# Kernel tuning notes

Hardware: AMD Instinct MI355X
Metric: run time of the kernel (lower is better)

The kernel has to match this reference:

```python
import jax, jax.numpy as jnp
import numpy as np

NCLASSES = 4
FG_THRESH = 0.5
MEANS = jnp.array([0.0, 0.0, 0.0, 0.0], dtype=jnp.float32)
STDS = jnp.array([0.1, 0.1, 0.2, 0.2], dtype=jnp.float32)
BBOX_INSIDE_W = jnp.array([1.0, 1.0, 1.0, 1.0], dtype=jnp.float32)


def _bbox_overlaps(boxes, gt):
    # boxes: (B,M,4), gt: (B,K,4) -> IoU (B,M,K), faithful to bbox_overlaps_batch
    aw = boxes[..., 2] - boxes[..., 0] + 1.0
    ah = boxes[..., 3] - boxes[..., 1] + 1.0
    gw = gt[..., 2] - gt[..., 0] + 1.0
    gh = gt[..., 3] - gt[..., 1] + 1.0
    area_a = aw * ah                      # (B,M)
    area_g = gw * gh                      # (B,K)
    ix1 = jnp.maximum(boxes[:, :, None, 0], gt[:, None, :, 0])
    iy1 = jnp.maximum(boxes[:, :, None, 1], gt[:, None, :, 1])
    ix2 = jnp.minimum(boxes[:, :, None, 2], gt[:, None, :, 2])
    iy2 = jnp.minimum(boxes[:, :, None, 3], gt[:, None, :, 3])
    iw = jnp.clip(ix2 - ix1 + 1.0, 0.0)
    ih = jnp.clip(iy2 - iy1 + 1.0, 0.0)
    inter = iw * ih                       # (B,M,K)
    ov = inter / (area_a[:, :, None] + area_g[:, None, :] - inter)
    gt_zero = (gw == 1.0) & (gh == 1.0)   # zero-area (padding) gt boxes
    an_zero = (aw == 1.0) & (ah == 1.0)
    ov = jnp.where(gt_zero[:, None, :], 0.0, ov)
    ov = jnp.where(an_zero[:, :, None], -1.0, ov)
    return ov


def _bbox_transform(ex, gt):
    ew = ex[..., 2] - ex[..., 0] + 1.0
    eh = ex[..., 3] - ex[..., 1] + 1.0
    ecx = ex[..., 0] + 0.5 * ew
    ecy = ex[..., 1] + 0.5 * eh
    gw = gt[..., 2] - gt[..., 0] + 1.0
    gh = gt[..., 3] - gt[..., 1] + 1.0
    gcx = gt[..., 0] + 0.5 * gw
    gcy = gt[..., 1] + 0.5 * gh
    dx = (gcx - ecx) / ew
    dy = (gcy - ecy) / eh
    dw = jnp.log(gw / ew)
    dh = jnp.log(gh / eh)
    return jnp.stack([dx, dy, dw, dh], axis=-1)


def setup_inputs() -> dict:
    key = jax.random.key(0)
    B, N, K = 16, 8192, 128
    ks = jax.random.split(key, 9)
    # valid proposal boxes inside an ~1242x375 (KITTI-like) image
    x1 = jax.random.uniform(ks[0], (B, N)) * 1000.0
    y1 = jax.random.uniform(ks[1], (B, N)) * 300.0
    bw = jax.random.uniform(ks[2], (B, N)) * 200.0 + 4.0
    bh = jax.random.uniform(ks[3], (B, N)) * 150.0 + 4.0
    all_rois = jnp.concatenate(
        [jnp.zeros((B, N, 1), jnp.float32),
         jnp.stack([x1, y1, x1 + bw, y1 + bh], axis=-1)], axis=-1)
    gx1 = jax.random.uniform(ks[4], (B, K)) * 1000.0
    gy1 = jax.random.uniform(ks[5], (B, K)) * 300.0
    gw = jax.random.uniform(ks[6], (B, K)) * 200.0 + 8.0
    gh = jax.random.uniform(ks[7], (B, K)) * 150.0 + 8.0
    cls = jax.random.randint(ks[8], (B, K), 1, NCLASSES).astype(jnp.float32)
    gt_boxes = jnp.stack([gx1, gy1, gx1 + gw, gy1 + gh, cls], axis=-1)
    return {"all_rois": all_rois, "gt_boxes": gt_boxes}


def reference(all_rois, gt_boxes):
    B = all_rois.shape[0]
    dt = all_rois.dtype
    # append gt boxes as extra rois: (0, x1, y1, x2, y2)
    gt_append = jnp.concatenate(
        [jnp.zeros_like(gt_boxes[..., :1]), gt_boxes[..., :4]], axis=-1)
    rois = jnp.concatenate([all_rois, gt_append], axis=1)   # (B,M,5)
    M = rois.shape[1]

    ov = _bbox_overlaps(rois[..., 1:5], gt_boxes[..., :4])  # (B,M,K)
    max_ov = ov.max(axis=2)                                 # (B,M)
    gt_assign = jnp.argmax(ov, axis=2)                      # (B,M)
    labels_all = jnp.take_along_axis(gt_boxes[..., 4], gt_assign, axis=1)

    # focal-loss path: fg = ov >= thresh, keep order = [fg asc, bg asc]
    fg = max_ov >= FG_THRESH
    order = jnp.argsort(jnp.where(fg, 0, 1).astype(jnp.int32), axis=1, stable=True)
    fg_count = fg.sum(axis=1)                               # (B,)
    pos = jnp.arange(M)[None, :]

    labels_perm = jnp.take_along_axis(labels_all, order, axis=1)
    labels_batch = jnp.where(pos < fg_count[:, None], labels_perm, 0.0)

    rois_perm = jnp.take_along_axis(rois, order[..., None], axis=1)
    rois_batch = rois_perm.at[..., 0].set(
        jnp.broadcast_to(jnp.arange(B, dtype=dt)[:, None], (B, M)))

    ga_perm = jnp.take_along_axis(gt_assign, order, axis=1)
    gt_rois = jnp.take_along_axis(gt_boxes, ga_perm[..., None], axis=1)  # (B,M,5)

    targets = _bbox_transform(rois_batch[..., 1:5], gt_rois[..., :4])
    targets = (targets - MEANS) / STDS
    bbox_targets = jnp.where((labels_batch > 0)[..., None], targets, 0.0)

    # focal inside weights in ORIGINAL roi order (as in the source), bg zeroed
    focal_w = jnp.where(fg, (1.0 - max_ov) ** 2, 0.0)       # (B,M)
    bbox_inside_weights = jnp.broadcast_to(focal_w[..., None], (B, M, 4))
    bbox_outside_weights = (bbox_inside_weights > 0).astype(dt)

    return (rois_batch, labels_batch, bbox_targets,
            bbox_inside_weights, bbox_outside_weights)
```

## Files before the change

### kernel.cpp

```cpp
#include <hip/hip_runtime.h>
#include <math.h>

#define BB 16
#define NN 8192
#define KK 128
#define MM (NN + KK)
#define NCHUNK ((MM + 255) / 256)

__global__ __launch_bounds__(256) void ptl_phase1(
    const float* __restrict__ all_rois,
    const float* __restrict__ gt_boxes,
    int* __restrict__ fg_flags,
    int* __restrict__ gt_assign,
    int* __restrict__ chunk_counts,
    float* __restrict__ out_inside,
    float* __restrict__ out_outside)
{
    __shared__ float4 s_box[KK];
    __shared__ int    s_wcnt[4];

    const int b   = blockIdx.y;
    const int tid = threadIdx.x;

    if (tid < KK) {
        const float* g = gt_boxes + ((size_t)b * KK + tid) * 5;
        float gx1 = g[0], gy1 = g[1], gx2 = g[2], gy2 = g[3];
        float gw = gx2 - gx1 + 1.0f, gh = gy2 - gy1 + 1.0f;
        bool z = (gw == 1.0f) && (gh == 1.0f);
        s_box[tid] = z ? make_float4(1e30f, 1e30f, -1e30f, -1e30f)
                       : make_float4(gx1, gy1, gx2 + 1.0f, gy2 + 1.0f);
    }
    __syncthreads();

    const int i = blockIdx.x * 256 + tid;
    const bool valid = (i < MM);

    float x1 = 0.f, y1 = 0.f, x2 = 0.f, y2 = 0.f;
    if (valid) {
        if (i < NN) {
            const float* p = all_rois + ((size_t)b * NN + i) * 5;
            x1 = p[1]; y1 = p[2]; x2 = p[3]; y2 = p[4];
        } else {
            const float* p = gt_boxes + ((size_t)b * KK + (i - NN)) * 5;
            x1 = p[0]; y1 = p[1]; x2 = p[2]; y2 = p[3];
        }
    }
    const float X2p = x2 + 1.0f, Y2p = y2 + 1.0f;
    const float aw = X2p - x1, ah = Y2p - y1;
    const float area_a = aw * ah;

    float best = -1e30f;
    int besti = 0;
    #pragma unroll 4
    for (int k = 0; k < KK; ++k) {
        float4 g = s_box[k];
        float iw = fmaxf(fminf(X2p, g.z) - fmaxf(x1, g.x), 0.0f);
        float ih = fmaxf(fminf(Y2p, g.w) - fmaxf(y1, g.y), 0.0f);
        float inter = iw * ih;
        float area_g = (g.z - g.x) * (g.w - g.y);
        float ov = inter / (area_a + area_g - inter);
        if (ov > best) { best = ov; besti = k; }
    }
    if (aw == 1.0f && ah == 1.0f) { best = -1.0f; besti = 0; }

    const bool fg = valid && (best >= 0.5f);

    unsigned long long m = __ballot(fg ? 1 : 0);
    if ((tid & 63) == 0) s_wcnt[tid >> 6] = __popcll(m);
    __syncthreads();
    if (tid == 0)
        chunk_counts[b * NCHUNK + blockIdx.x] =
            s_wcnt[0] + s_wcnt[1] + s_wcnt[2] + s_wcnt[3];

    if (!valid) return;
    const size_t idx = (size_t)b * MM + i;
    fg_flags[idx]  = fg ? 1 : 0;
    gt_assign[idx] = besti;

    const float om = 1.0f - best;
    const float w  = fg ? om * om : 0.0f;
    const float ow = (w > 0.0f) ? 1.0f : 0.0f;
    ((float4*)out_inside)[idx]  = make_float4(w, w, w, w);
    ((float4*)out_outside)[idx] = make_float4(ow, ow, ow, ow);
}

__global__ __launch_bounds__(256) void ptl_phase2(
    const float* __restrict__ all_rois,
    const float* __restrict__ gt_boxes,
    const int* __restrict__ fg_flags,
    const int* __restrict__ gt_assign,
    const int* __restrict__ chunk_counts,
    float* __restrict__ out_rois,
    float* __restrict__ out_labels,
    float* __restrict__ out_targets)
{
    __shared__ float s_gt[KK * 5];
    __shared__ int   s_cnt[NCHUNK];
    __shared__ int   s_w[4];

    const int b   = blockIdx.y;
    const int cx  = blockIdx.x;
    const int tid = threadIdx.x;

    for (int t = tid; t < KK * 5; t += 256)
        s_gt[t] = gt_boxes[(size_t)b * KK * 5 + t];
    if (tid < NCHUNK)
        s_cnt[tid] = chunk_counts[b * NCHUNK + tid];
    __syncthreads();

    int base = 0, total = 0;
    for (int c = 0; c < NCHUNK; ++c) {
        int v = s_cnt[c];
        total += v;
        if (c < cx) base += v;
    }

    const int i = cx * 256 + tid;
    const bool valid = (i < MM);
    int f = 0, a = 0;
    if (valid) {
        const size_t idx = (size_t)b * MM + i;
        f = fg_flags[idx];
        a = gt_assign[idx];
    }

    const int lane = tid & 63, wv = tid >> 6;
    unsigned long long m = __ballot(f);
    const int lp = __popcll(m & ((1ull << lane) - 1ull));
    if (lane == 0) s_w[wv] = __popcll(m);
    __syncthreads();
    int we = 0;
    for (int w2 = 0; w2 < wv; ++w2) we += s_w[w2];
    const int fgBefore = base + we + lp;

    if (!valid) return;
    const int p = f ? fgBefore : (total + i - fgBefore);

    float x1, y1, x2, y2;
    if (i < NN) {
        const float* q = all_rois + ((size_t)b * NN + i) * 5;
        x1 = q[1]; y1 = q[2]; x2 = q[3]; y2 = q[4];
    } else {
        const float* q = gt_boxes + ((size_t)b * KK + (i - NN)) * 5;
        x1 = q[0]; y1 = q[1]; x2 = q[2]; y2 = q[3];
    }

    float* rp = out_rois + ((size_t)b * MM + p) * 5;
    rp[0] = (float)b;
    rp[1] = x1; rp[2] = y1; rp[3] = x2; rp[4] = y2;

    float lbl = 0.f, t0 = 0.f, t1 = 0.f, t2 = 0.f, t3 = 0.f;
    if (f) {
        lbl = s_gt[a * 5 + 4];
        if (lbl > 0.0f) {
            const float gx1 = s_gt[a * 5 + 0], gy1 = s_gt[a * 5 + 1];
            const float gx2 = s_gt[a * 5 + 2], gy2 = s_gt[a * 5 + 3];
            const float ew = x2 - x1 + 1.0f, eh = y2 - y1 + 1.0f;
            const float ecx = x1 + 0.5f * ew, ecy = y1 + 0.5f * eh;
            const float gw = gx2 - gx1 + 1.0f, gh = gy2 - gy1 + 1.0f;
            const float gcx = gx1 + 0.5f * gw, gcy = gy1 + 0.5f * gh;
            t0 = ((gcx - ecx) / ew) / 0.1f;
            t1 = ((gcy - ecy) / eh) / 0.1f;
            t2 = logf(gw / ew) / 0.2f;
            t3 = logf(gh / eh) / 0.2f;
        }
    }
    out_labels[(size_t)b * MM + p] = lbl;
    float* tp = out_targets + ((size_t)b * MM + p) * 4;
    tp[0] = t0; tp[1] = t1; tp[2] = t2; tp[3] = t3;
}

extern "C" void kernel_launch(void* const* d_in, const int* in_sizes, int n_in,
                              void* d_out, int out_size, void* d_ws, size_t ws_size,
                              hipStream_t stream) {
    const float* all_rois = (const float*)d_in[0];
    const float* gt_boxes = (const float*)d_in[1];

    float* out = (float*)d_out;
    float* out_rois    = out;
    float* out_labels  = out_rois    + (size_t)BB * MM * 5;
    float* out_targets = out_labels  + (size_t)BB * MM;
    float* out_inside  = out_targets + (size_t)BB * MM * 4;
    float* out_outside = out_inside  + (size_t)BB * MM * 4;

    int* fg_flags     = (int*)d_ws;
    int* gt_assign    = fg_flags  + (size_t)BB * MM;
    int* chunk_counts = gt_assign + (size_t)BB * MM;

    dim3 grid(NCHUNK, BB);
    ptl_phase1<<<grid, 256, 0, stream>>>(all_rois, gt_boxes, fg_flags, gt_assign,
                                         chunk_counts, out_inside, out_outside);
    ptl_phase2<<<grid, 256, 0, stream>>>(all_rois, gt_boxes, fg_flags, gt_assign,
                                         chunk_counts, out_rois, out_labels,
                                         out_targets);
}
```

Measured before the change: 83.30 us.

## Fuse IoU/assignment and compaction phases into one cooperative kernel with grid sync

Merges the two kernels into a single cooperative launch that uses a grid-wide barrier between computing per-chunk foreground counts and doing the compacted scatter. Each thread keeps its box coordinates, best IoU and assigned gt index in registers across the barrier. This removes the fg_flags and gt_assign workspace round trip, the second read of the ROIs and gt boxes, and one kernel launch. In exchange it pays for a grid sync and depends on all 528 blocks being co-resident, which cooperative launch enforces.

```diff
diff --git a/kernel.cpp b/kernel.cpp
--- a/kernel.cpp
+++ b/kernel.cpp
@@ -1,4 +1,5 @@
 #include <hip/hip_runtime.h>
+#include <hip/hip_cooperative_groups.h>
 #include <math.h>
 
 #define BB 16
@@ -7,19 +8,25 @@
 #define MM (NN + KK)
 #define NCHUNK ((MM + 255) / 256)
 
-__global__ __launch_bounds__(256) void ptl_phase1(
+namespace cg = cooperative_groups;
+
+__global__ __launch_bounds__(256) void ptl_fused(
     const float* __restrict__ all_rois,
     const float* __restrict__ gt_boxes,
-    int* __restrict__ fg_flags,
-    int* __restrict__ gt_assign,
     int* __restrict__ chunk_counts,
+    float* __restrict__ out_rois,
+    float* __restrict__ out_labels,
+    float* __restrict__ out_targets,
     float* __restrict__ out_inside,
     float* __restrict__ out_outside)
 {
     __shared__ float4 s_box[KK];
-    __shared__ int    s_wcnt[4];
+    __shared__ float  s_lbl[KK];
+    __shared__ int    s_w[4];
+    __shared__ int    s_cnt[NCHUNK];
 
     const int b   = blockIdx.y;
+    const int cx  = blockIdx.x;
     const int tid = threadIdx.x;
 
     if (tid < KK) {
@@ -29,10 +36,11 @@
         bool z = (gw == 1.0f) && (gh == 1.0f);
         s_box[tid] = z ? make_float4(1e30f, 1e30f, -1e30f, -1e30f)
                        : make_float4(gx1, gy1, gx2 + 1.0f, gy2 + 1.0f);
+        s_lbl[tid] = g[4];
     }
     __syncthreads();
 
-    const int i = blockIdx.x * 256 + tid;
+    const int i = cx * 256 + tid;
     const bool valid = (i < MM);
 
     float x1 = 0.f, y1 = 0.f, x2 = 0.f, y2 = 0.f;
@@ -65,49 +73,36 @@
 
     const bool fg = valid && (best >= 0.5f);
 
+    const int lane = tid & 63, wv = tid >> 6;
     unsigned long long m = __ballot(fg ? 1 : 0);
-    if ((tid & 63) == 0) s_wcnt[tid >> 6] = __popcll(m);
+    const int lp = __popcll(m & ((1ull << lane) - 1ull));
+    if (lane == 0) s_w[wv] = __popcll(m);
     __syncthreads();
-    if (tid == 0)
-        chunk_counts[b * NCHUNK + blockIdx.x] =
-            s_wcnt[0] + s_wcnt[1] + s_wcnt[2] + s_wcnt[3];
+    if (tid == 0) {
+        int s = s_w[0] + s_w[1] + s_w[2] + s_w[3];
+        __hip_atomic_store(&chunk_counts[b * NCHUNK + cx], s,
+                           __ATOMIC_RELAXED, __HIP_MEMORY_SCOPE_AGENT);
+    }
+    int we = 0;
+    for (int w2 = 0; w2 < wv; ++w2) we += s_w[w2];
+    const int inChunkExcl = we + lp;
 
-    if (!valid) return;
-    const size_t idx = (size_t)b * MM + i;
-    fg_flags[idx]  = fg ? 1 : 0;
-    gt_assign[idx] = besti;
+    if (valid) {
+        const size_t idx = (size_t)b * MM + i;
+        const float om = 1.0f - best;
+        const float w  = fg ? om * om : 0.0f;
+        const float ow = (w > 0.0f) ? 1.0f : 0.0f;
+        ((float4*)out_inside)[idx]  = make_float4(w, w, w, w);
+        ((float4*)out_outside)[idx] = make_float4(ow, ow, ow, ow);
+    }
 
-    const float om = 1.0f - best;
-    const float w  = fg ? om * om : 0.0f;
-    const float ow = (w > 0.0f) ? 1.0f : 0.0f;
-    ((float4*)out_inside)[idx]  = make_float4(w, w, w, w);
-    ((float4*)out_outside)[idx] = make_float4(ow, ow, ow, ow);
-}
+    __threadfence();
+    cg::this_grid().sync();
 
-__global__ __launch_bounds__(256) void ptl_phase2(
-    const float* __restrict__ all_rois,
-    const float* __restrict__ gt_boxes,
-    const int* __restrict__ fg_flags,
-    const int* __restrict__ gt_assign,
-    const int* __restrict__ chunk_counts,
-    float* __restrict__ out_rois,
-    float* __restrict__ out_labels,
-    float* __restrict__ out_targets)
-{
-    __shared__ float s_gt[KK * 5];
-    __shared__ int   s_cnt[NCHUNK];
-    __shared__ int   s_w[4];
-
-    const int b   = blockIdx.y;
-    const int cx  = blockIdx.x;
-    const int tid = threadIdx.x;
-
-    for (int t = tid; t < KK * 5; t += 256)
-        s_gt[t] = gt_boxes[(size_t)b * KK * 5 + t];
     if (tid < NCHUNK)
-        s_cnt[tid] = chunk_counts[b * NCHUNK + tid];
+        s_cnt[tid] = __hip_atomic_load(&chunk_counts[b * NCHUNK + tid],
+                                       __ATOMIC_RELAXED, __HIP_MEMORY_SCOPE_AGENT);
     __syncthreads();
-
     int base = 0, total = 0;
     for (int c = 0; c < NCHUNK; ++c) {
         int v = s_cnt[c];
@@ -115,50 +110,23 @@
         if (c < cx) base += v;
     }
 
-    const int i = cx * 256 + tid;
-    const bool valid = (i < MM);
-    int f = 0, a = 0;
-    if (valid) {
-        const size_t idx = (size_t)b * MM + i;
-        f = fg_flags[idx];
-        a = gt_assign[idx];
-    }
-
-    const int lane = tid & 63, wv = tid >> 6;
-    unsigned long long m = __ballot(f);
-    const int lp = __popcll(m & ((1ull << lane) - 1ull));
-    if (lane == 0) s_w[wv] = __popcll(m);
-    __syncthreads();
-    int we = 0;
-    for (int w2 = 0; w2 < wv; ++w2) we += s_w[w2];
-    const int fgBefore = base + we + lp;
-
     if (!valid) return;
-    const int p = f ? fgBefore : (total + i - fgBefore);
-
-    float x1, y1, x2, y2;
-    if (i < NN) {
-        const float* q = all_rois + ((size_t)b * NN + i) * 5;
-        x1 = q[1]; y1 = q[2]; x2 = q[3]; y2 = q[4];
-    } else {
-        const float* q = gt_boxes + ((size_t)b * KK + (i - NN)) * 5;
-        x1 = q[0]; y1 = q[1]; x2 = q[2]; y2 = q[3];
-    }
+    const int fgBefore = base + inChunkExcl;
+    const int p = fg ? fgBefore : (total + i - fgBefore);
 
     float* rp = out_rois + ((size_t)b * MM + p) * 5;
     rp[0] = (float)b;
     rp[1] = x1; rp[2] = y1; rp[3] = x2; rp[4] = y2;
 
     float lbl = 0.f, t0 = 0.f, t1 = 0.f, t2 = 0.f, t3 = 0.f;
-    if (f) {
-        lbl = s_gt[a * 5 + 4];
+    if (fg) {
+        lbl = s_lbl[besti];
         if (lbl > 0.0f) {
-            const float gx1 = s_gt[a * 5 + 0], gy1 = s_gt[a * 5 + 1];
-            const float gx2 = s_gt[a * 5 + 2], gy2 = s_gt[a * 5 + 3];
+            float4 g = s_box[besti];
+            const float gw = g.z - g.x, gh = g.w - g.y;
+            const float gcx = g.x + 0.5f * gw, gcy = g.y + 0.5f * gh;
             const float ew = x2 - x1 + 1.0f, eh = y2 - y1 + 1.0f;
             const float ecx = x1 + 0.5f * ew, ecy = y1 + 0.5f * eh;
-            const float gw = gx2 - gx1 + 1.0f, gh = gy2 - gy1 + 1.0f;
-            const float gcx = gx1 + 0.5f * gw, gcy = gy1 + 0.5f * gh;
             t0 = ((gcx - ecx) / ew) / 0.1f;
             t1 = ((gcy - ecy) / eh) / 0.1f;
             t2 = logf(gw / ew) / 0.2f;
@@ -183,14 +151,14 @@
     float* out_inside  = out_targets + (size_t)BB * MM * 4;
     float* out_outside = out_inside  + (size_t)BB * MM * 4;
 
-    int* fg_flags     = (int*)d_ws;
-    int* gt_assign    = fg_flags  + (size_t)BB * MM;
-    int* chunk_counts = gt_assign + (size_t)BB * MM;
+    int* chunk_counts = (int*)d_ws;
 
-    dim3 grid(NCHUNK, BB);
-    ptl_phase1<<<grid, 256, 0, stream>>>(all_rois, gt_boxes, fg_flags, gt_assign,
-                                         chunk_counts, out_inside, out_outside);
-    ptl_phase2<<<grid, 256, 0, stream>>>(all_rois, gt_boxes, fg_flags, gt_assign,
-                                         chunk_counts, out_rois, out_labels,
-                                         out_targets);
+    void* args[] = {
+        (void*)&all_rois, (void*)&gt_boxes, (void*)&chunk_counts,
+        (void*)&out_rois, (void*)&out_labels, (void*)&out_targets,
+        (void*)&out_inside, (void*)&out_outside
+    };
+    hipLaunchCooperativeKernel((const void*)ptl_fused,
+                               dim3(NCHUNK, BB), dim3(256, 1, 1),
+                               args, 0, stream);
 }
```

Measured after the change: 194.1 us. 133% more time.
